# Kernel tuning notes

Hardware: AMD Instinct MI355X
Metric: run time of the kernel (lower is better)

## Reference

```python
import jax, jax.numpy as jnp
import numpy as np
from jax.scipy.special import logsumexp

N_NODES = 20000
N_FEAT = 64
N_TPL = 10
TPL_NODES = 10
K_NEIGH = 15  # local neighborhood cap -> local graph size kloc = K+1 (self first)
N_EDGES = N_NODES * 16


def setup_inputs() -> dict:
    key = jax.random.key(0)
    k1, k2, k3, k4, k5 = jax.random.split(key, 5)
    x = jax.random.normal(k1, (N_NODES, N_FEAT), dtype=jnp.float32)
    edge_index = jax.random.randint(k2, (2, N_EDGES), 0, N_NODES, dtype=jnp.int32)
    # template_initialisation: randint{0,1} adjacency + N(0, 0.01) noise
    adj = jax.random.randint(k3, (N_TPL, TPL_NODES, TPL_NODES), 0, 2).astype(jnp.float32)
    templates = adj + 0.01 * jax.random.normal(k4, (N_TPL, TPL_NODES, TPL_NODES), dtype=jnp.float32)
    # template features ~ N(0.0012, 0.02)
    templates_features = 0.0012 + 0.02 * jax.random.normal(
        k5, (N_TPL, TPL_NODES, N_FEAT), dtype=jnp.float32)
    alpha0 = jnp.array([0.5], dtype=jnp.float32)
    return {"x": x, "edge_index": edge_index, "templates": templates,
            "templates_features": templates_features, "alpha0": alpha0}


def _fgw_distances(x, edge_index, templates, templates_features, alpha0,
                   K=K_NEIGH, n_outer=3, n_sink=5):
    """Per-node fused GW distance between the node's local (star) subgraph and
    each learned template, solved with an entropic proximal / Sinkhorn scheme.
    Returns [N, T]."""
    N, F = x.shape
    Tn, n, _ = templates.shape
    kloc = K + 1

    # ---- build fixed-size neighbor lists from edge_index (int ops, constant) ----
    src, dst = edge_index[0], edge_index[1]
    E = src.shape[0]
    order = jnp.argsort(src)
    src_s, dst_s = src[order], dst[order]
    deg = jnp.zeros((N,), jnp.int32).at[src].add(1)
    start = jnp.cumsum(deg) - deg                       # CSR row starts
    rank = jnp.arange(E, dtype=jnp.int32) - start[src_s]  # position within each node's list
    # rank >= K falls out of bounds -> dropped
    neigh = jnp.zeros((N, K), jnp.int32).at[src_s, rank].set(dst_s, mode="drop")
    nb_mask = (jnp.arange(K)[None, :] < jnp.minimum(deg, K)[:, None]).astype(x.dtype)  # [N,K]

    # ---- local graphs: self node first, then up to K neighbors ----
    xloc = jnp.concatenate([x[:, None, :], x[neigh]], axis=1)  # [N, kloc, F]
    m = jnp.concatenate([jnp.ones((N, 1), x.dtype), nb_mask], axis=1)  # [N, kloc]
    p = m / jnp.sum(m, -1, keepdims=True)                # node-side marginal
    q = jnp.full((n,), 1.0 / n, x.dtype)                 # template-side marginal

    # star adjacency of the 1-hop neighborhood
    row0 = jnp.concatenate([jnp.zeros((N, 1), x.dtype), nb_mask], axis=1)
    C1 = jnp.zeros((N, kloc, kloc), x.dtype).at[:, 0, :].set(row0).at[:, :, 0].set(row0)
    C2 = templates  # [T, n, n]

    # feature cost M[n_node, t, k, m] = ||xloc - y||^2
    M = (jnp.sum(xloc ** 2, -1)[:, None, :, None]
         + jnp.sum(templates_features ** 2, -1)[None, :, None, :]
         - 2.0 * jnp.einsum("nkf,tmf->ntkm", xloc, templates_features))

    alpha = jax.nn.sigmoid(alpha0)[0]

    # GW square-loss constant terms (Peyre et al. trick)
    hC1 = jnp.einsum("nkl,nl->nk", C1 ** 2, p)   # [N, kloc]
    hC2 = jnp.einsum("tmr,r->tm", C2 ** 2, q)    # [T, n]
    constC = hC1[:, None, :, None] + hC2[None, :, None, :]

    def gw_tens(Tp):  # Tp: [N, T, kloc, n]
        tmp = jnp.einsum("nkl,ntlm->ntkm", C1, Tp)
        return constC - 2.0 * jnp.einsum("ntkm,trm->ntkr", tmp, C2)

    eps = 0.05 * jax.lax.stop_gradient(jnp.mean(M)) + 1e-6
    logp = jnp.where(m > 0, jnp.log(jnp.maximum(p, 1e-30)), -1e9)[:, None, :]  # [N,1,kloc]
    logq = jnp.log(q)  # [n]

    Tp = p[:, None, :, None] * q[None, None, None, :]  # independent-coupling init
    f = jnp.zeros((N, Tn, kloc), x.dtype)
    g = jnp.zeros((N, Tn, n), x.dtype)
    for _ in range(n_outer):  # outer FGW linearization steps
        G = (1.0 - alpha) * M + 2.0 * alpha * gw_tens(Tp)
        logK = -G / eps
        for _ in range(n_sink):  # log-domain Sinkhorn on linearized cost
            f = eps * (logp - logsumexp(logK + g[:, :, None, :] / eps, axis=-1))
            g = eps * (logq - logsumexp(logK + f[:, :, :, None] / eps, axis=-2))
        Tp = jnp.exp(logK + f[:, :, :, None] / eps + g[:, :, None, :] / eps)

    dist = ((1.0 - alpha) * jnp.sum(M * Tp, axis=(-2, -1))
            + alpha * jnp.sum(gw_tens(Tp) * Tp, axis=(-2, -1)))
    return dist  # [N, T]


def reference(x, edge_index, templates, templates_features, alpha0):
    return _fgw_distances(x, edge_index, templates, templates_features, alpha0)
```

## Files before the change

### kernel.cpp

```cpp
#include <hip/hip_runtime.h>

#define N_NODES 20000
#define NPAIRS  10000
#define N_EDGES 320000
#define CAP     64
#define KN      15
#define GRID_MAIN 2500

typedef _Float16 half_t;
typedef _Float16 half2_t __attribute__((ext_vector_type(2)));
typedef _Float16 half8_t __attribute__((ext_vector_type(8)));

#define P_ALPHA 0
#define P_BETA  1
#define P_IEPS2 2
#define P_EPS   3
#define P_HC2   16
#define P_RSC2  216
#define P_F1    316

#define OFF_CNT    0u
#define OFF_S2X    80000u
#define OFF_STATS  160000u
#define OFF_FLAG   160520u
#define OFF_NBC    160528u
#define OFF_NEIGH  240528u
#define OFF_BUF    1440528u
#define OFF_PARAMS 6560528u
#define MEMSET_LEN 160528u

#define TF_STRIDE 648

template<int CTRL>
__device__ __forceinline__ float dpp_add(float v) {
  int s = __builtin_bit_cast(int, v);
  int r = __builtin_amdgcn_update_dpp(0, s, CTRL, 0xF, 0xF, true);
  return v + __builtin_bit_cast(float, r);
}
__device__ __forceinline__ float sum16(float v) {
  v = dpp_add<0x128>(v);
  v = dpp_add<0x124>(v);
  v = dpp_add<0x122>(v);
  v = dpp_add<0x121>(v);
  return v;
}
__device__ __forceinline__ float bcast16(float v) {
  return __builtin_bit_cast(float,
      __builtin_amdgcn_ds_swizzle(__builtin_bit_cast(int, v), 0x010));
}
__device__ __forceinline__ float fdot2(half2_t a, half2_t b, float c) {
  return __builtin_amdgcn_fdot2(a, b, c, false);
}
__device__ __forceinline__ half2_t h2(unsigned int u) {
  return __builtin_bit_cast(half2_t, u);
}
__device__ __forceinline__ float sgpr(float v) {
  return __builtin_bit_cast(float,
      __builtin_amdgcn_readfirstlane(__builtin_bit_cast(int, v)));
}

__global__ void k_scatter(const int* __restrict__ ei, int* __restrict__ cnt,
                          int* __restrict__ buf) {
  int e = blockIdx.x * blockDim.x + threadIdx.x;
  if (e >= N_EDGES) return;
  int s = ei[e];
  int slot = atomicAdd(&cnt[s], 1);
  if (slot < CAP) buf[s * CAP + slot] = e;
}

#define SS_BLOCKS 1250
__global__ void __launch_bounds__(256)
k_selstats(const int* __restrict__ ei, const int* __restrict__ cnt,
           const int* __restrict__ buf, const float* __restrict__ x,
           int* __restrict__ nbc_g, int* __restrict__ neigh,
           float* __restrict__ s2xh, double* __restrict__ stats,
           int* __restrict__ flag,
           const float* __restrict__ tf, const float* __restrict__ c2,
           const float* __restrict__ alpha0, float* __restrict__ params) {
  const int lane = threadIdx.x & 63;
  const int wid = threadIdx.x >> 6;
  const int* dst = ei + N_EDGES;
  const float x0 = x[lane];
  const float x0sq = x0 * x0;
  float accx = 0.f, acc2 = 0.f;
  __shared__ int dsh[4][16];

  for (int w = blockIdx.x * 4 + wid; w < N_NODES; w += SS_BLOCKS * 4) {
    int c = cnt[w];
    int cc = c < CAP ? c : CAP;
    int e = (lane < cc) ? buf[w * CAP + lane] : 0x7fffffff;
    int nb = c < KN ? c : KN;
    bool sel;
    if (cc <= KN) {
      sel = lane < cc;
    } else {
      int rank = 0;
      for (int j = 0; j < cc; j++) {
        int ej = __shfl(e, j);
        rank += (ej < e) ? 1 : 0;
      }
      sel = (e != 0x7fffffff) && (rank < KN);
    }
    unsigned long long mask = __ballot(sel);
    int d = sel ? dst[e] : 0;
    if (sel) {
      int pos = __popcll(mask & ((1ull << lane) - 1ull));
      neigh[w * KN + pos] = d;
      dsh[wid][pos] = d;
    }
    if (lane == 0) nbc_g[w] = nb;

    float sv = x[w * 64 + lane];
    {
      float hv = (float)(half_t)sv;
      float sq = hv * hv;
#pragma unroll
      for (int off = 32; off > 0; off >>= 1) sq += __shfl_xor(sq, off, 64);
      if (lane == 0) s2xh[w] = sq;
    }
    float ax = sv, a2 = sv * sv;
    int idx[KN];
#pragma unroll
    for (int r = 0; r < KN; r++) idx[r] = dsh[wid][r];
#pragma unroll
    for (int r = 0; r < KN; r++) {
      if (r < nb) {
        float nv = x[(size_t)idx[r] * 64 + lane];
        ax += nv;
        a2 = fmaf(nv, nv, a2);
      }
    }
    float w0 = (float)(KN - nb);
    ax = fmaf(w0, x0, ax);
    a2 = fmaf(w0, x0sq, a2);
    accx += ax;
    acc2 += a2;
  }

#pragma unroll
  for (int off = 32; off > 0; off >>= 1) acc2 += __shfl_xor(acc2, off, 64);
  __shared__ float redx[4][64];
  __shared__ float red2[4];
  __shared__ int lastsh;
  redx[wid][lane] = accx;
  if (lane == 0) red2[wid] = acc2;
  __syncthreads();
  int tid = threadIdx.x;
  if (tid < 64) {
    float s = redx[0][tid] + redx[1][tid] + redx[2][tid] + redx[3][tid];
    atomicAdd(&stats[1 + tid], (double)s);
  }
  if (tid == 0)
    atomicAdd(&stats[0], (double)(red2[0] + red2[1] + red2[2] + red2[3]));
  __syncthreads();
  if (tid == 0) {
    __threadfence();
    int old = atomicAdd(flag, 1);
    lastsh = (old == SS_BLOCKS - 1) ? 1 : 0;
  }
  __syncthreads();
  if (!lastsh) return;
  __threadfence();
  __shared__ float sh[4];
  if (tid < 64) {
    float s = 0.f, s2 = 0.f;
    for (int tm = 0; tm < 100; tm++) { float v = tf[tm * 64 + tid]; s += v; s2 += v * v; }
    double inv16N = 1.0 / (double)(N_NODES * 16);
    double cross = (stats[1 + tid] * inv16N) * ((double)s / 100.0);
    double B = (double)s2 / 100.0;
    double term = B - 2.0 * cross;
#pragma unroll
    for (int off = 32; off > 0; off >>= 1) term += __shfl_xor(term, off, 64);
    if (tid == 0) {
      double A = stats[0] * inv16N;
      double meanM = A + term;
      float eps = (float)(0.05 * meanM) + 1e-6f;
      float a0 = alpha0[0];
      float alpha = 1.f / (1.f + expf(-a0));
      params[P_ALPHA] = alpha;
      params[P_BETA]  = 1.f - alpha;
      params[P_IEPS2] = 1.4426950408889634f / eps;
      params[P_EPS]   = eps;
      sh[0] = alpha; sh[1] = 1.f - alpha; sh[2] = 1.4426950408889634f / eps;
    }
  }
  __syncthreads();
  if (tid < 100) {
    float alpha = sh[0], beta = sh[1], ieps2 = sh[2];
    int t = tid / 10, mm = tid % 10;
    float h = 0.f;
    for (int r = 0; r < 10; r++) { float cv = c2[t * 100 + mm * 10 + r]; h += cv * cv; }
    float hc2v = 0.1f * h;
    params[P_HC2 + tid] = hc2v;
    float s2 = 0.f;
    for (int f = 0; f < 64; f++) { float v = tf[tid * 64 + f]; s2 += v * v; }
    float rs = 0.f;
    for (int m2_ = 0; m2_ < 10; m2_++) rs += c2[t * 100 + mm * 10 + m2_];
    params[P_RSC2 + tid] = rs;
    params[P_F1 + tid] = (beta * s2 + 2.0f * alpha * hc2v) * (-ieps2);
  }
}

__global__ void __launch_bounds__(256)
k_xhalf(const float* __restrict__ x, half_t* __restrict__ xh) {
  int i = (blockIdx.x * 256 + threadIdx.x) * 8;
  float4 a = *(const float4*)(x + i);
  float4 b = *(const float4*)(x + i + 4);
  half8_t h = { (half_t)a.x, (half_t)a.y, (half_t)a.z, (half_t)a.w,
                (half_t)b.x, (half_t)b.y, (half_t)b.z, (half_t)b.w };
  *(half8_t*)(xh + i) = h;
}

__global__ void __launch_bounds__(320, 6)
k_main(const half_t* __restrict__ xh, const float* __restrict__ tf_g,
       const float* __restrict__ c2_g, const int* __restrict__ nbc_g,
       const int* __restrict__ neigh_g, const float* __restrict__ params,
       const float* __restrict__ s2x_g, float* __restrict__ out) {
  __shared__ __align__(16) half_t tf_l[10 * TF_STRIDE];
  __shared__ __align__(16) float c2_l[1000];
  __shared__ __align__(16) float hc2_l[100];
  __shared__ __align__(16) float rsc2_l[100];
  __shared__ __align__(16) float F1_l[100];
  __shared__ __align__(16) float bsb_l[20][10][2];

  const int tid = threadIdx.x;
  const int node_s = tid / 160;
  const int s = tid % 160;
  const int t = s >> 4;
  const int k = s & 15;
  const bool k0 = (k == 0);
  const int grp = node_s * 10 + t;

  for (int i = tid; i < 6400; i += 320) {
    int tt = i / 640, rem = i - tt * 640;
    tf_l[tt * TF_STRIDE + rem] = (half_t)tf_g[i];
  }
  for (int i = tid; i < 1000; i += 320) c2_l[i] = c2_g[i];
  if (tid < 100) {
    hc2_l[tid]  = params[P_HC2 + tid];
    rsc2_l[tid] = params[P_RSC2 + tid];
    F1_l[tid]   = params[P_F1 + tid];
  }

  const float alpha = sgpr(params[P_ALPHA]);
  const float beta  = sgpr(params[P_BETA]);
  const float ieps2 = sgpr(params[P_IEPS2]);
  const float eps   = sgpr(params[P_EPS]);
  const float niep  = -ieps2;
  const float twoal = 2.0f * alpha;
  const float ctv10 = 0.2f * twoal * ieps2;
  const float cab   = 2.0f * beta * ieps2;
  const float c_a2d = -eps * 0.69314718056f;
  const float twoal01 = 0.1f * twoal;

  const int idx_c2 = t * 100 + ((k < 10) ? k : 9) * 10;
  __syncthreads();

  const int kk = (k == 0) ? 0 : (k - 1);
  const half_t* tfb = &tf_l[t * TF_STRIDE];
  int p = blockIdx.x;
  int nb_pf = nbc_g[2 * p + node_s];
  int nbr_pf = neigh_g[(2 * p + node_s) * KN + kk];

#pragma unroll 1
  for (; p < NPAIRS; p += gridDim.x) {
    const int v = 2 * p + node_s;
    const int nb = nb_pf;
    const int srcn = (k == 0) ? v : (kk < nb ? nbr_pf : 0);
    const float s2x = s2x_g[srcn];
    const uint4* xr = (const uint4*)(xh + (size_t)srcn * 64);

    uint4 q[8];
#pragma unroll
    for (int r = 0; r < 8; r++) q[r] = xr[r];

    {
      int vn = 2 * (p + gridDim.x) + node_s;
      vn = vn < N_NODES ? vn : 0;
      nb_pf = nbc_g[vn];
      nbr_pf = neigh_g[vn * KN + kk];
    }

    float acc[10];
#pragma unroll
    for (int m = 0; m < 10; m++) {
      float a = 0.0f;
#pragma unroll
      for (int ch = 0; ch < 4; ch++) {
        uint4 tqa = *(const uint4*)&tfb[m * 64 + ch * 16];
        uint4 tqb = *(const uint4*)&tfb[m * 64 + ch * 16 + 8];
        const uint4 qa = q[2 * ch];
        const uint4 qb = q[2 * ch + 1];
        a = fdot2(h2(tqa.x), h2(qa.x), a);
        a = fdot2(h2(tqa.y), h2(qa.y), a);
        a = fdot2(h2(tqa.z), h2(qa.z), a);
        a = fdot2(h2(tqa.w), h2(qa.w), a);
        a = fdot2(h2(tqb.x), h2(qb.x), a);
        a = fdot2(h2(tqb.y), h2(qb.y), a);
        a = fdot2(h2(tqb.z), h2(qb.z), a);
        a = fdot2(h2(tqb.w), h2(qb.w), a);
      }
      acc[m] = a;
    }

    const float inv = 1.0f / (float)(1 + nb);
    const float pk = (k <= nb) ? inv : 0.0f;
    const float hC1k = (k == 0) ? (float)nb * inv : ((k <= nb) ? inv : 0.0f);
    const float base = (beta * s2x + twoal * hC1k) * niep;
    const float ctm  = ctv10 * ((k == 0) ? (float)nb * inv : inv);

    float Ab[10];
#pragma unroll
    for (int j = 0; j < 5; j++) {
      float2 f1v = *(const float2*)&F1_l[t * 10 + 2 * j];
      Ab[2 * j]     = fmaf(cab, acc[2 * j],     f1v.x + base);
      Ab[2 * j + 1] = fmaf(cab, acc[2 * j + 1], f1v.y + base);
    }

    float K[10], vv[10];
    float u = 1.0f;
#pragma unroll
    for (int m = 0; m < 10; m++) vv[m] = 1.0f;

#pragma unroll
    for (int j = 0; j < 5; j++) {
      float2 rs = *(const float2*)&rsc2_l[t * 10 + 2 * j];
      K[2 * j]     = __builtin_amdgcn_exp2f(fmaf(ctm, rs.x, Ab[2 * j]));
      K[2 * j + 1] = __builtin_amdgcn_exp2f(fmaf(ctm, rs.y, Ab[2 * j + 1]));
    }

#pragma unroll 1
    for (int o = 0; o < 3; o++) {
#pragma unroll 1
      for (int it = 0; it < 5; it++) {
        float kv0 = 0.0f, kv1 = 0.0f;
#pragma unroll
        for (int m = 0; m < 10; m += 2) {
          kv0 = fmaf(K[m],     vv[m],     kv0);
          kv1 = fmaf(K[m + 1], vv[m + 1], kv1);
        }
        u = pk * __builtin_amdgcn_rcpf(kv0 + kv1);
#pragma unroll
        for (int m = 0; m < 10; m++) {
          float w = sum16(K[m] * u);
          vv[m] = __builtin_amdgcn_rcpf(w);
        }
      }
      if (o == 2) break;
      {
        float B = 0.0f, SB = 0.0f;
#pragma unroll
        for (int j = 0; j < 5; j++) {
          float2 c2p = *(const float2*)&c2_l[idx_c2 + 2 * j];
          float tka = K[2 * j] * vv[2 * j] * u;
          float tkb = K[2 * j + 1] * vv[2 * j + 1] * u;
          B  = fmaf(bcast16(tka), c2p.x, B);
          SB = fmaf(sum16(tka),   c2p.x, SB);
          B  = fmaf(bcast16(tkb), c2p.y, B);
          SB = fmaf(sum16(tkb),   c2p.y, SB);
        }
        if (k < 10) { bsb_l[grp][k][0] = B; bsb_l[grp][k][1] = SB; }
        __threadfence_block();
#pragma unroll
        for (int j = 0; j < 5; j++) {
          float4 bv = *(const float4*)&bsb_l[grp][2 * j][0];
          float tva = k0 ? (bv.y - bv.x) : bv.x;
          float tvb = k0 ? (bv.w - bv.z) : bv.z;
          K[2 * j]     = __builtin_amdgcn_exp2f(fmaf(ctv10, tva, Ab[2 * j]));
          K[2 * j + 1] = __builtin_amdgcn_exp2f(fmaf(ctv10, tvb, Ab[2 * j + 1]));
        }
        __threadfence_block();
      }
    }

    {
      float tk[10];
      float B = 0.0f, SB = 0.0f;
#pragma unroll
      for (int j = 0; j < 5; j++) {
        float2 c2p = *(const float2*)&c2_l[idx_c2 + 2 * j];
        tk[2 * j]     = K[2 * j] * vv[2 * j] * u;
        tk[2 * j + 1] = K[2 * j + 1] * vv[2 * j + 1] * u;
        B  = fmaf(bcast16(tk[2 * j]), c2p.x, B);
        SB = fmaf(sum16(tk[2 * j]),   c2p.x, SB);
        B  = fmaf(bcast16(tk[2 * j + 1]), c2p.y, B);
        SB = fmaf(sum16(tk[2 * j + 1]),   c2p.y, SB);
      }
      if (k < 10) { bsb_l[grp][k][0] = B; bsb_l[grp][k][1] = SB; }
      __threadfence_block();
      float dd = 0.0f;
#pragma unroll
      for (int j = 0; j < 5; j++) {
        float4 bv = *(const float4*)&bsb_l[grp][2 * j][0];
        float2 h2v = *(const float2*)&hc2_l[t * 10 + 2 * j];
        float tva = k0 ? (bv.y - bv.x) : bv.x;
        float tvb = k0 ? (bv.w - bv.z) : bv.z;
        float c1a = fmaf(alpha, hC1k + h2v.x, twoal01 * tva);
        float c1b = fmaf(alpha, hC1k + h2v.y, twoal01 * tvb);
        float coa = fmaf(c_a2d, Ab[2 * j], -c1a);
        float cob = fmaf(c_a2d, Ab[2 * j + 1], -c1b);
        dd = fmaf(coa, tk[2 * j], dd);
        dd = fmaf(cob, tk[2 * j + 1], dd);
      }
      __threadfence_block();
      dd = sum16(dd * 0.1f);
      if (k == 0) out[v * 10 + t] = dd;
    }
  }
}

extern "C" void kernel_launch(void* const* d_in, const int* in_sizes, int n_in,
                              void* d_out, int out_size, void* d_ws, size_t ws_size,
                              hipStream_t stream) {
  const float* x  = (const float*)d_in[0];
  const int*   ei = (const int*)d_in[1];
  const float* c2 = (const float*)d_in[2];
  const float* tf = (const float*)d_in[3];
  const float* a0 = (const float*)d_in[4];
  float* out = (float*)d_out;
  char* ws = (char*)d_ws;
  int*    cnt    = (int*)(ws + OFF_CNT);
  float*  s2xh   = (float*)(ws + OFF_S2X);
  double* stats  = (double*)(ws + OFF_STATS);
  int*    flag   = (int*)(ws + OFF_FLAG);
  int*    nbc    = (int*)(ws + OFF_NBC);
  int*    neigh  = (int*)(ws + OFF_NEIGH);
  int*    buf    = (int*)(ws + OFF_BUF);
  half_t* xhalf  = (half_t*)(ws + OFF_BUF);
  float*  params = (float*)(ws + OFF_PARAMS);
  (void)in_sizes; (void)n_in; (void)out_size; (void)ws_size;

  hipMemsetAsync(ws, 0, MEMSET_LEN, stream);
  k_scatter<<<N_EDGES / 256, 256, 0, stream>>>(ei, cnt, buf);
  k_selstats<<<SS_BLOCKS, 256, 0, stream>>>(ei, cnt, buf, x, nbc, neigh,
                                            s2xh, stats, flag, tf, c2, a0, params);
  k_xhalf<<<625, 256, 0, stream>>>(x, xhalf);
  k_main<<<GRID_MAIN, 320, 0, stream>>>(xhalf, tf, c2, nbc, neigh, params, s2xh, out);
}
```

Baseline: 393.2 us.

## Interleave two node pairs per thread for instruction-level parallelism in Sinkhorn loop

Each thread now processes two independent node pairs (A and B) at once, interleaving their dot products, Sinkhorn iterations and cross-lane reductions so that dependent latency chains (rcp, DPP sums, exp2) can overlap. The loop is fixed at two iterations over pair indices derived from a hard-coded grid of 2500, and the shared scratch is doubled. Register use roughly doubles, so the occupancy hint drops from 6 to 3 blocks, trading thread-level for instruction-level parallelism.

```diff
diff --git a/kernel.cpp b/kernel.cpp
--- a/kernel.cpp
+++ b/kernel.cpp
@@ -211,7 +211,7 @@
   *(half8_t*)(xh + i) = h;
 }
 
-__global__ void __launch_bounds__(320, 6)
+__global__ void __launch_bounds__(320, 3)
 k_main(const half_t* __restrict__ xh, const float* __restrict__ tf_g,
        const float* __restrict__ c2_g, const int* __restrict__ nbc_g,
        const int* __restrict__ neigh_g, const float* __restrict__ params,
@@ -221,7 +221,7 @@
   __shared__ __align__(16) float hc2_l[100];
   __shared__ __align__(16) float rsc2_l[100];
   __shared__ __align__(16) float F1_l[100];
-  __shared__ __align__(16) float bsb_l[20][10][2];
+  __shared__ __align__(16) float bsb_l[2][20][10][2];
 
   const int tid = threadIdx.x;
   const int node_s = tid / 160;
@@ -258,153 +258,222 @@
 
   const int kk = (k == 0) ? 0 : (k - 1);
   const half_t* tfb = &tf_l[t * TF_STRIDE];
-  int p = blockIdx.x;
-  int nb_pf = nbc_g[2 * p + node_s];
-  int nbr_pf = neigh_g[(2 * p + node_s) * KN + kk];
+
+  int nbA_pf  = nbc_g[2 * blockIdx.x + node_s];
+  int nbrA_pf = neigh_g[(2 * blockIdx.x + node_s) * KN + kk];
+  int nbB_pf  = nbc_g[2 * (blockIdx.x + 2500) + node_s];
+  int nbrB_pf = neigh_g[(2 * (blockIdx.x + 2500) + node_s) * KN + kk];
 
 #pragma unroll 1
-  for (; p < NPAIRS; p += gridDim.x) {
-    const int v = 2 * p + node_s;
-    const int nb = nb_pf;
-    const int srcn = (k == 0) ? v : (kk < nb ? nbr_pf : 0);
-    const float s2x = s2x_g[srcn];
-    const uint4* xr = (const uint4*)(xh + (size_t)srcn * 64);
-
-    uint4 q[8];
-#pragma unroll
-    for (int r = 0; r < 8; r++) q[r] = xr[r];
+  for (int ii = 0; ii < 2; ii++) {
+    const int pA = blockIdx.x + ii * 5000;
+    const int pB = pA + 2500;
+    const int vA = 2 * pA + node_s;
+    const int vB = 2 * pB + node_s;
+    const int nbA = nbA_pf, nbB = nbB_pf;
+    const int srcA = k0 ? vA : (kk < nbA ? nbrA_pf : 0);
+    const int srcB = k0 ? vB : (kk < nbB ? nbrB_pf : 0);
+    const float s2xA = s2x_g[srcA];
+    const float s2xB = s2x_g[srcB];
+    const uint4* xrA = (const uint4*)(xh + (size_t)srcA * 64);
+    const uint4* xrB = (const uint4*)(xh + (size_t)srcB * 64);
+
+    uint4 qA[8], qB[8];
+#pragma unroll
+    for (int r = 0; r < 8; r++) { qA[r] = xrA[r]; qB[r] = xrB[r]; }
 
     {
-      int vn = 2 * (p + gridDim.x) + node_s;
-      vn = vn < N_NODES ? vn : 0;
-      nb_pf = nbc_g[vn];
-      nbr_pf = neigh_g[vn * KN + kk];
-    }
-
-    float acc[10];
+      int vAn = 2 * (pA + 5000) + node_s; vAn = vAn < N_NODES ? vAn : 0;
+      int vBn = 2 * (pB + 5000) + node_s; vBn = vBn < N_NODES ? vBn : 0;
+      nbA_pf = nbc_g[vAn];  nbrA_pf = neigh_g[vAn * KN + kk];
+      nbB_pf = nbc_g[vBn];  nbrB_pf = neigh_g[vBn * KN + kk];
+    }
+
+    float accA[10], accB[10];
 #pragma unroll
     for (int m = 0; m < 10; m++) {
-      float a = 0.0f;
+      float a = 0.0f, b = 0.0f;
 #pragma unroll
       for (int ch = 0; ch < 4; ch++) {
         uint4 tqa = *(const uint4*)&tfb[m * 64 + ch * 16];
         uint4 tqb = *(const uint4*)&tfb[m * 64 + ch * 16 + 8];
-        const uint4 qa = q[2 * ch];
-        const uint4 qb = q[2 * ch + 1];
+        const uint4 qa = qA[2 * ch];
+        const uint4 qb = qA[2 * ch + 1];
+        const uint4 ra = qB[2 * ch];
+        const uint4 rb = qB[2 * ch + 1];
         a = fdot2(h2(tqa.x), h2(qa.x), a);
+        b = fdot2(h2(tqa.x), h2(ra.x), b);
         a = fdot2(h2(tqa.y), h2(qa.y), a);
+        b = fdot2(h2(tqa.y), h2(ra.y), b);
         a = fdot2(h2(tqa.z), h2(qa.z), a);
+        b = fdot2(h2(tqa.z), h2(ra.z), b);
         a = fdot2(h2(tqa.w), h2(qa.w), a);
+        b = fdot2(h2(tqa.w), h2(ra.w), b);
         a = fdot2(h2(tqb.x), h2(qb.x), a);
+        b = fdot2(h2(tqb.x), h2(rb.x), b);
         a = fdot2(h2(tqb.y), h2(qb.y), a);
+        b = fdot2(h2(tqb.y), h2(rb.y), b);
         a = fdot2(h2(tqb.z), h2(qb.z), a);
+        b = fdot2(h2(tqb.z), h2(rb.z), b);
         a = fdot2(h2(tqb.w), h2(qb.w), a);
-      }
-      acc[m] = a;
-    }
-
-    const float inv = 1.0f / (float)(1 + nb);
-    const float pk = (k <= nb) ? inv : 0.0f;
-    const float hC1k = (k == 0) ? (float)nb * inv : ((k <= nb) ? inv : 0.0f);
-    const float base = (beta * s2x + twoal * hC1k) * niep;
-    const float ctm  = ctv10 * ((k == 0) ? (float)nb * inv : inv);
-
-    float Ab[10];
+        b = fdot2(h2(tqb.w), h2(rb.w), b);
+      }
+      accA[m] = a;
+      accB[m] = b;
+    }
+
+    const float invA = 1.0f / (float)(1 + nbA);
+    const float invB = 1.0f / (float)(1 + nbB);
+    const float pkA = (k <= nbA) ? invA : 0.0f;
+    const float pkB = (k <= nbB) ? invB : 0.0f;
+    const float hC1kA = (k == 0) ? (float)nbA * invA : ((k <= nbA) ? invA : 0.0f);
+    const float hC1kB = (k == 0) ? (float)nbB * invB : ((k <= nbB) ? invB : 0.0f);
+    const float baseA = (beta * s2xA + twoal * hC1kA) * niep;
+    const float baseB = (beta * s2xB + twoal * hC1kB) * niep;
+    const float ctmA  = ctv10 * ((k == 0) ? (float)nbA * invA : invA);
+    const float ctmB  = ctv10 * ((k == 0) ? (float)nbB * invB : invB);
+
+    float AbA[10], AbB[10];
 #pragma unroll
     for (int j = 0; j < 5; j++) {
       float2 f1v = *(const float2*)&F1_l[t * 10 + 2 * j];
-      Ab[2 * j]     = fmaf(cab, acc[2 * j],     f1v.x + base);
-      Ab[2 * j + 1] = fmaf(cab, acc[2 * j + 1], f1v.y + base);
-    }
-
-    float K[10], vv[10];
-    float u = 1.0f;
-#pragma unroll
-    for (int m = 0; m < 10; m++) vv[m] = 1.0f;
+      AbA[2 * j]     = fmaf(cab, accA[2 * j],     f1v.x + baseA);
+      AbB[2 * j]     = fmaf(cab, accB[2 * j],     f1v.x + baseB);
+      AbA[2 * j + 1] = fmaf(cab, accA[2 * j + 1], f1v.y + baseA);
+      AbB[2 * j + 1] = fmaf(cab, accB[2 * j + 1], f1v.y + baseB);
+    }
+
+    float KA[10], KB[10], vvA[10], vvB[10];
+    float uA = 1.0f, uB = 1.0f;
+#pragma unroll
+    for (int m = 0; m < 10; m++) { vvA[m] = 1.0f; vvB[m] = 1.0f; }
 
 #pragma unroll
     for (int j = 0; j < 5; j++) {
       float2 rs = *(const float2*)&rsc2_l[t * 10 + 2 * j];
-      K[2 * j]     = __builtin_amdgcn_exp2f(fmaf(ctm, rs.x, Ab[2 * j]));
-      K[2 * j + 1] = __builtin_amdgcn_exp2f(fmaf(ctm, rs.y, Ab[2 * j + 1]));
+      KA[2 * j]     = __builtin_amdgcn_exp2f(fmaf(ctmA, rs.x, AbA[2 * j]));
+      KB[2 * j]     = __builtin_amdgcn_exp2f(fmaf(ctmB, rs.x, AbB[2 * j]));
+      KA[2 * j + 1] = __builtin_amdgcn_exp2f(fmaf(ctmA, rs.y, AbA[2 * j + 1]));
+      KB[2 * j + 1] = __builtin_amdgcn_exp2f(fmaf(ctmB, rs.y, AbB[2 * j + 1]));
     }
 
 #pragma unroll 1
     for (int o = 0; o < 3; o++) {
 #pragma unroll 1
       for (int it = 0; it < 5; it++) {
-        float kv0 = 0.0f, kv1 = 0.0f;
+        float kvA0 = 0.0f, kvA1 = 0.0f, kvB0 = 0.0f, kvB1 = 0.0f;
 #pragma unroll
         for (int m = 0; m < 10; m += 2) {
-          kv0 = fmaf(K[m],     vv[m],     kv0);
-          kv1 = fmaf(K[m + 1], vv[m + 1], kv1);
+          kvA0 = fmaf(KA[m],     vvA[m],     kvA0);
+          kvB0 = fmaf(KB[m],     vvB[m],     kvB0);
+          kvA1 = fmaf(KA[m + 1], vvA[m + 1], kvA1);
+          kvB1 = fmaf(KB[m + 1], vvB[m + 1], kvB1);
         }
-        u = pk * __builtin_amdgcn_rcpf(kv0 + kv1);
+        uA = pkA * __builtin_amdgcn_rcpf(kvA0 + kvA1);
+        uB = pkB * __builtin_amdgcn_rcpf(kvB0 + kvB1);
 #pragma unroll
         for (int m = 0; m < 10; m++) {
-          float w = sum16(K[m] * u);
-          vv[m] = __builtin_amdgcn_rcpf(w);
+          float wA = sum16(KA[m] * uA);
+          float wB = sum16(KB[m] * uB);
+          vvA[m] = __builtin_amdgcn_rcpf(wA);
+          vvB[m] = __builtin_amdgcn_rcpf(wB);
         }
       }
       if (o == 2) break;
       {
-        float B = 0.0f, SB = 0.0f;
+        float BA = 0.0f, SBA = 0.0f, BB = 0.0f, SBB = 0.0f;
 #pragma unroll
         for (int j = 0; j < 5; j++) {
           float2 c2p = *(const float2*)&c2_l[idx_c2 + 2 * j];
-          float tka = K[2 * j] * vv[2 * j] * u;
-          float tkb = K[2 * j + 1] * vv[2 * j + 1] * u;
-          B  = fmaf(bcast16(tka), c2p.x, B);
-          SB = fmaf(sum16(tka),   c2p.x, SB);
-          B  = fmaf(bcast16(tkb), c2p.y, B);
-          SB = fmaf(sum16(tkb),   c2p.y, SB);
+          float tkaA = KA[2 * j] * vvA[2 * j] * uA;
+          float tkaB = KB[2 * j] * vvB[2 * j] * uB;
+          float tkbA = KA[2 * j + 1] * vvA[2 * j + 1] * uA;
+          float tkbB = KB[2 * j + 1] * vvB[2 * j + 1] * uB;
+          BA  = fmaf(bcast16(tkaA), c2p.x, BA);
+          BB  = fmaf(bcast16(tkaB), c2p.x, BB);
+          SBA = fmaf(sum16(tkaA),   c2p.x, SBA);
+          SBB = fmaf(sum16(tkaB),   c2p.x, SBB);
+          BA  = fmaf(bcast16(tkbA), c2p.y, BA);
+          BB  = fmaf(bcast16(tkbB), c2p.y, BB);
+          SBA = fmaf(sum16(tkbA),   c2p.y, SBA);
+          SBB = fmaf(sum16(tkbB),   c2p.y, SBB);
         }
-        if (k < 10) { bsb_l[grp][k][0] = B; bsb_l[grp][k][1] = SB; }
-        __threadfence_block();
-#pragma unroll
-        for (int j = 0; j < 5; j++) {
-          float4 bv = *(const float4*)&bsb_l[grp][2 * j][0];
-          float tva = k0 ? (bv.y - bv.x) : bv.x;
-          float tvb = k0 ? (bv.w - bv.z) : bv.z;
-          K[2 * j]     = __builtin_amdgcn_exp2f(fmaf(ctv10, tva, Ab[2 * j]));
-          K[2 * j + 1] = __builtin_amdgcn_exp2f(fmaf(ctv10, tvb, Ab[2 * j + 1]));
+        if (k < 10) {
+          bsb_l[0][grp][k][0] = BA; bsb_l[0][grp][k][1] = SBA;
+          bsb_l[1][grp][k][0] = BB; bsb_l[1][grp][k][1] = SBB;
         }
         __threadfence_block();
+#pragma unroll
+        for (int j = 0; j < 5; j++) {
+          float4 bvA = *(const float4*)&bsb_l[0][grp][2 * j][0];
+          float4 bvB = *(const float4*)&bsb_l[1][grp][2 * j][0];
+          float tvaA = k0 ? (bvA.y - bvA.x) : bvA.x;
+          float tvaB = k0 ? (bvB.y - bvB.x) : bvB.x;
+          float tvbA = k0 ? (bvA.w - bvA.z) : bvA.z;
+          float tvbB = k0 ? (bvB.w - bvB.z) : bvB.z;
+          KA[2 * j]     = __builtin_amdgcn_exp2f(fmaf(ctv10, tvaA, AbA[2 * j]));
+          KB[2 * j]     = __builtin_amdgcn_exp2f(fmaf(ctv10, tvaB, AbB[2 * j]));
+          KA[2 * j + 1] = __builtin_amdgcn_exp2f(fmaf(ctv10, tvbA, AbA[2 * j + 1]));
+          KB[2 * j + 1] = __builtin_amdgcn_exp2f(fmaf(ctv10, tvbB, AbB[2 * j + 1]));
+        }
+        __threadfence_block();
       }
     }
 
     {
-      float tk[10];
-      float B = 0.0f, SB = 0.0f;
+      float tkA[10], tkB[10];
+      float BA = 0.0f, SBA = 0.0f, BB = 0.0f, SBB = 0.0f;
 #pragma unroll
       for (int j = 0; j < 5; j++) {
         float2 c2p = *(const float2*)&c2_l[idx_c2 + 2 * j];
-        tk[2 * j]     = K[2 * j] * vv[2 * j] * u;
-        tk[2 * j + 1] = K[2 * j + 1] * vv[2 * j + 1] * u;
-        B  = fmaf(bcast16(tk[2 * j]), c2p.x, B);
-        SB = fmaf(sum16(tk[2 * j]),   c2p.x, SB);
-        B  = fmaf(bcast16(tk[2 * j + 1]), c2p.y, B);
-        SB = fmaf(sum16(tk[2 * j + 1]),   c2p.y, SB);
-      }
-      if (k < 10) { bsb_l[grp][k][0] = B; bsb_l[grp][k][1] = SB; }
+        tkA[2 * j]     = KA[2 * j] * vvA[2 * j] * uA;
+        tkB[2 * j]     = KB[2 * j] * vvB[2 * j] * uB;
+        tkA[2 * j + 1] = KA[2 * j + 1] * vvA[2 * j + 1] * uA;
+        tkB[2 * j + 1] = KB[2 * j + 1] * vvB[2 * j + 1] * uB;
+        BA  = fmaf(bcast16(tkA[2 * j]), c2p.x, BA);
+        BB  = fmaf(bcast16(tkB[2 * j]), c2p.x, BB);
+        SBA = fmaf(sum16(tkA[2 * j]),   c2p.x, SBA);
+        SBB = fmaf(sum16(tkB[2 * j]),   c2p.x, SBB);
+        BA  = fmaf(bcast16(tkA[2 * j + 1]), c2p.y, BA);
+        BB  = fmaf(bcast16(tkB[2 * j + 1]), c2p.y, BB);
+        SBA = fmaf(sum16(tkA[2 * j + 1]),   c2p.y, SBA);
+        SBB = fmaf(sum16(tkB[2 * j + 1]),   c2p.y, SBB);
+      }
+      if (k < 10) {
+        bsb_l[0][grp][k][0] = BA; bsb_l[0][grp][k][1] = SBA;
+        bsb_l[1][grp][k][0] = BB; bsb_l[1][grp][k][1] = SBB;
+      }
       __threadfence_block();
-      float dd = 0.0f;
+      float ddA = 0.0f, ddB = 0.0f;
 #pragma unroll
       for (int j = 0; j < 5; j++) {
-        float4 bv = *(const float4*)&bsb_l[grp][2 * j][0];
+        float4 bvA = *(const float4*)&bsb_l[0][grp][2 * j][0];
+        float4 bvB = *(const float4*)&bsb_l[1][grp][2 * j][0];
         float2 h2v = *(const float2*)&hc2_l[t * 10 + 2 * j];
-        float tva = k0 ? (bv.y - bv.x) : bv.x;
-        float tvb = k0 ? (bv.w - bv.z) : bv.z;
-        float c1a = fmaf(alpha, hC1k + h2v.x, twoal01 * tva);
-        float c1b = fmaf(alpha, hC1k + h2v.y, twoal01 * tvb);
-        float coa = fmaf(c_a2d, Ab[2 * j], -c1a);
-        float cob = fmaf(c_a2d, Ab[2 * j + 1], -c1b);
-        dd = fmaf(coa, tk[2 * j], dd);
-        dd = fmaf(cob, tk[2 * j + 1], dd);
+        float tvaA = k0 ? (bvA.y - bvA.x) : bvA.x;
+        float tvaB = k0 ? (bvB.y - bvB.x) : bvB.x;
+        float tvbA = k0 ? (bvA.w - bvA.z) : bvA.z;
+        float tvbB = k0 ? (bvB.w - bvB.z) : bvB.z;
+        float c1aA = fmaf(alpha, hC1kA + h2v.x, twoal01 * tvaA);
+        float c1aB = fmaf(alpha, hC1kB + h2v.x, twoal01 * tvaB);
+        float c1bA = fmaf(alpha, hC1kA + h2v.y, twoal01 * tvbA);
+        float c1bB = fmaf(alpha, hC1kB + h2v.y, twoal01 * tvbB);
+        float coaA = fmaf(c_a2d, AbA[2 * j], -c1aA);
+        float coaB = fmaf(c_a2d, AbB[2 * j], -c1aB);
+        float cobA = fmaf(c_a2d, AbA[2 * j + 1], -c1bA);
+        float cobB = fmaf(c_a2d, AbB[2 * j + 1], -c1bB);
+        ddA = fmaf(coaA, tkA[2 * j], ddA);
+        ddB = fmaf(coaB, tkB[2 * j], ddB);
+        ddA = fmaf(cobA, tkA[2 * j + 1], ddA);
+        ddB = fmaf(cobB, tkB[2 * j + 1], ddB);
       }
       __threadfence_block();
-      dd = sum16(dd * 0.1f);
-      if (k == 0) out[v * 10 + t] = dd;
+      ddA = sum16(ddA * 0.1f);
+      ddB = sum16(ddB * 0.1f);
+      if (k == 0) {
+        out[vA * 10 + t] = ddA;
+        out[vB * 10 + t] = ddB;
+      }
     }
   }
 }
```

After: 421.1 us. 7.1% more time.

## Replace neighbor-gather stats with per-node occurrence counts and fuse half conversion

Applied to the files above, without the earlier changes.

The selection kernel no longer gathers neighbor feature rows to build global mean statistics. It instead counts with atomics how often each node appears as a neighbor, plus the padding count. A new pass kernel then streams x once, weighting each row by its count, and also writes the half-precision copy and squared norms, which removes the separate conversion kernel. It also lowers the scatter cap from 64 to 48 and fully unrolls the inner Sinkhorn loop. The trade-off is extra atomic traffic on the count array, an added memset, and a pass kernel launched with only 200 blocks.

```diff
diff --git a/kernel.cpp b/kernel.cpp
--- a/kernel.cpp
+++ b/kernel.cpp
@@ -3,13 +3,12 @@
 #define N_NODES 20000
 #define NPAIRS  10000
 #define N_EDGES 320000
-#define CAP     64
+#define CAP     48
 #define KN      15
 #define GRID_MAIN 2500
 
 typedef _Float16 half_t;
 typedef _Float16 half2_t __attribute__((ext_vector_type(2)));
-typedef _Float16 half8_t __attribute__((ext_vector_type(8)));
 
 #define P_ALPHA 0
 #define P_BETA  1
@@ -23,9 +22,11 @@
 #define OFF_S2X    80000u
 #define OFF_STATS  160000u
 #define OFF_FLAG   160520u
+#define OFF_PAD    160524u
 #define OFF_NBC    160528u
 #define OFF_NEIGH  240528u
 #define OFF_BUF    1440528u
+#define OFF_WCT    5280528u
 #define OFF_PARAMS 6560528u
 #define MEMSET_LEN 160528u
 
@@ -70,20 +71,17 @@
 
 #define SS_BLOCKS 1250
 __global__ void __launch_bounds__(256)
-k_selstats(const int* __restrict__ ei, const int* __restrict__ cnt,
-           const int* __restrict__ buf, const float* __restrict__ x,
-           int* __restrict__ nbc_g, int* __restrict__ neigh,
-           float* __restrict__ s2xh, double* __restrict__ stats,
-           int* __restrict__ flag,
-           const float* __restrict__ tf, const float* __restrict__ c2,
-           const float* __restrict__ alpha0, float* __restrict__ params) {
+k_sel(const int* __restrict__ ei, const int* __restrict__ cnt,
+      const int* __restrict__ buf, int* __restrict__ nbc_g,
+      int* __restrict__ neigh, int* __restrict__ wct,
+      int* __restrict__ padc) {
   const int lane = threadIdx.x & 63;
   const int wid = threadIdx.x >> 6;
   const int* dst = ei + N_EDGES;
-  const float x0 = x[lane];
-  const float x0sq = x0 * x0;
-  float accx = 0.f, acc2 = 0.f;
-  __shared__ int dsh[4][16];
+  __shared__ int padsh;
+  if (threadIdx.x == 0) padsh = 0;
+  __syncthreads();
+  int padacc = 0;
 
   for (int w = blockIdx.x * 4 + wid; w < N_NODES; w += SS_BLOCKS * 4) {
     int c = cnt[w];
@@ -102,39 +100,45 @@
       sel = (e != 0x7fffffff) && (rank < KN);
     }
     unsigned long long mask = __ballot(sel);
-    int d = sel ? dst[e] : 0;
     if (sel) {
       int pos = __popcll(mask & ((1ull << lane) - 1ull));
+      int d = dst[e];
       neigh[w * KN + pos] = d;
-      dsh[wid][pos] = d;
-    }
-    if (lane == 0) nbc_g[w] = nb;
-
-    float sv = x[w * 64 + lane];
-    {
-      float hv = (float)(half_t)sv;
-      float sq = hv * hv;
-#pragma unroll
-      for (int off = 32; off > 0; off >>= 1) sq += __shfl_xor(sq, off, 64);
-      if (lane == 0) s2xh[w] = sq;
-    }
-    float ax = sv, a2 = sv * sv;
-    int idx[KN];
-#pragma unroll
-    for (int r = 0; r < KN; r++) idx[r] = dsh[wid][r];
-#pragma unroll
-    for (int r = 0; r < KN; r++) {
-      if (r < nb) {
-        float nv = x[(size_t)idx[r] * 64 + lane];
-        ax += nv;
-        a2 = fmaf(nv, nv, a2);
-      }
-    }
-    float w0 = (float)(KN - nb);
-    ax = fmaf(w0, x0, ax);
-    a2 = fmaf(w0, x0sq, a2);
-    accx += ax;
-    acc2 += a2;
+      atomicAdd(&wct[d], 1);
+    }
+    if (lane == 0) { nbc_g[w] = nb; padacc += KN - nb; }
+  }
+  if (lane == 0 && padacc) atomicAdd(&padsh, padacc);
+  __syncthreads();
+  if (threadIdx.x == 0 && padsh) atomicAdd(padc, padsh);
+}
+
+#define PB 200
+__global__ void __launch_bounds__(256)
+k_pass(const float* __restrict__ x, half_t* __restrict__ xh,
+       const int* __restrict__ wct, const int* __restrict__ padc,
+       float* __restrict__ s2xh, double* __restrict__ stats,
+       int* __restrict__ flag, const float* __restrict__ tf,
+       const float* __restrict__ c2, const float* __restrict__ alpha0,
+       float* __restrict__ params) {
+  const int lane = threadIdx.x & 63;
+  const int wid = threadIdx.x >> 6;
+  const int tid = threadIdx.x;
+  const int pad = *padc;
+  float accx = 0.f, acc2 = 0.f;
+
+  for (int n = blockIdx.x * 4 + wid; n < N_NODES; n += PB * 4) {
+    float xv = x[n * 64 + lane];
+    half_t hv = (half_t)xv;
+    xh[n * 64 + lane] = hv;
+    float hf = (float)hv;
+    float sq = hf * hf;
+#pragma unroll
+    for (int off = 32; off > 0; off >>= 1) sq += __shfl_xor(sq, off, 64);
+    if (lane == 0) s2xh[n] = sq;
+    float wt = (float)(1 + wct[n] + ((n == 0) ? pad : 0));
+    accx = fmaf(wt, xv, accx);
+    acc2 = fmaf(wt, xv * xv, acc2);
   }
 
 #pragma unroll
@@ -145,7 +149,6 @@
   redx[wid][lane] = accx;
   if (lane == 0) red2[wid] = acc2;
   __syncthreads();
-  int tid = threadIdx.x;
   if (tid < 64) {
     float s = redx[0][tid] + redx[1][tid] + redx[2][tid] + redx[3][tid];
     atomicAdd(&stats[1 + tid], (double)s);
@@ -156,7 +159,7 @@
   if (tid == 0) {
     __threadfence();
     int old = atomicAdd(flag, 1);
-    lastsh = (old == SS_BLOCKS - 1) ? 1 : 0;
+    lastsh = (old == PB - 1) ? 1 : 0;
   }
   __syncthreads();
   if (!lastsh) return;
@@ -201,16 +204,6 @@
   }
 }
 
-__global__ void __launch_bounds__(256)
-k_xhalf(const float* __restrict__ x, half_t* __restrict__ xh) {
-  int i = (blockIdx.x * 256 + threadIdx.x) * 8;
-  float4 a = *(const float4*)(x + i);
-  float4 b = *(const float4*)(x + i + 4);
-  half8_t h = { (half_t)a.x, (half_t)a.y, (half_t)a.z, (half_t)a.w,
-                (half_t)b.x, (half_t)b.y, (half_t)b.z, (half_t)b.w };
-  *(half8_t*)(xh + i) = h;
-}
-
 __global__ void __launch_bounds__(320, 6)
 k_main(const half_t* __restrict__ xh, const float* __restrict__ tf_g,
        const float* __restrict__ c2_g, const int* __restrict__ nbc_g,
@@ -331,7 +324,7 @@
 
 #pragma unroll 1
     for (int o = 0; o < 3; o++) {
-#pragma unroll 1
+#pragma unroll
       for (int it = 0; it < 5; it++) {
         float kv0 = 0.0f, kv1 = 0.0f;
 #pragma unroll
@@ -423,17 +416,20 @@
   float*  s2xh   = (float*)(ws + OFF_S2X);
   double* stats  = (double*)(ws + OFF_STATS);
   int*    flag   = (int*)(ws + OFF_FLAG);
+  int*    padc   = (int*)(ws + OFF_PAD);
   int*    nbc    = (int*)(ws + OFF_NBC);
   int*    neigh  = (int*)(ws + OFF_NEIGH);
   int*    buf    = (int*)(ws + OFF_BUF);
   half_t* xhalf  = (half_t*)(ws + OFF_BUF);
+  int*    wct    = (int*)(ws + OFF_WCT);
   float*  params = (float*)(ws + OFF_PARAMS);
   (void)in_sizes; (void)n_in; (void)out_size; (void)ws_size;
 
   hipMemsetAsync(ws, 0, MEMSET_LEN, stream);
+  hipMemsetAsync(ws + OFF_WCT, 0, 80000, stream);
   k_scatter<<<N_EDGES / 256, 256, 0, stream>>>(ei, cnt, buf);
-  k_selstats<<<SS_BLOCKS, 256, 0, stream>>>(ei, cnt, buf, x, nbc, neigh,
-                                            s2xh, stats, flag, tf, c2, a0, params);
-  k_xhalf<<<625, 256, 0, stream>>>(x, xhalf);
+  k_sel<<<SS_BLOCKS, 256, 0, stream>>>(ei, cnt, buf, nbc, neigh, wct, padc);
+  k_pass<<<PB, 256, 0, stream>>>(x, xhalf, wct, padc, s2xh, stats, flag,
+                                 tf, c2, a0, params);
   k_main<<<GRID_MAIN, 320, 0, stream>>>(xhalf, tf, c2, nbc, neigh, params, s2xh, out);
 }
```

After: 381.9 us. -2.9%, faster.
